# Kernel tuning notes

Measured on AMD Instinct MI355X. Metric: run time of the kernel, lower is better.

## Reference

```python
import jax, jax.numpy as jnp
import numpy as np
from jax import lax

EPS = 1e-5  # nn.BatchNorm2d default eps


def _binarize_act(x):
    # out = sign(x).detach() - clip(x).detach() + clip(x)  (STE)
    c = jnp.clip(x, -1.0, 1.0)
    return c + lax.stop_gradient(jnp.sign(x) - c)


def _binarize_weight(w):
    # w.data = w.fp.sign().add(0.01).sign()  -> {-1,+1}, zeros map to +1.
    # Autograd in torch sees identity wrt the parameter (data swap), i.e. STE.
    wb = jnp.sign(jnp.sign(w) + 0.01)
    return w + lax.stop_gradient(wb - w)


def setup_inputs() -> dict:
    key = jax.random.key(0)
    k1, k2, k3, k4 = jax.random.split(key, 4)
    N, Cin, Cout, H, W = 16, 32, 32, 256, 256
    return {
        "x": jax.random.normal(k1, (N, Cin, H, W), dtype=jnp.float32),
        "weight": jax.random.normal(k2, (Cout, Cin, 3, 3), dtype=jnp.float32),
        "gamma": jnp.ones((Cout,), dtype=jnp.float32),
        "beta": jnp.zeros((Cout,), dtype=jnp.float32),
        "running_mean": jax.random.normal(k3, (Cout,), dtype=jnp.float32) * 0.1,
        "running_var": jax.random.uniform(k4, (Cout,), dtype=jnp.float32) + 0.5,
    }


def reference(x, weight, gamma, beta, running_mean, running_var):
    xb = _binarize_act(x)
    wb = _binarize_weight(weight)
    # 3x3, stride 1, padding 1 -> SAME spatial size
    out = lax.conv_general_dilated(
        xb, wb,
        window_strides=(1, 1),
        padding=((1, 1), (1, 1)),
        dimension_numbers=("NCHW", "OIHW", "NCHW"),
    )
    # BatchNorm2d (inference form with running stats), then ReLU
    inv = gamma / jnp.sqrt(running_var + EPS)  # [C]
    out = out * inv[None, :, None, None] + (beta - running_mean * inv)[None, :, None, None]
    return jax.nn.relu(out)
```

## Files before the change

kernel.cpp:

```cpp
#include <hip/hip_runtime.h>
#include <stdint.h>

#define NB   16
#define CIN  32
#define COUT 32
#define HH   256
#define WW   256
#define HWSZ (HH * WW)
#define EPSV 1e-5f
#define TWD  264

typedef int v4i  __attribute__((ext_vector_type(4)));
typedef int v16i __attribute__((ext_vector_type(16)));

__global__ __launch_bounds__(288) void pack_w_kernel(
    const float* __restrict__ wt, const float* __restrict__ gamma,
    const float* __restrict__ beta, const float* __restrict__ rmean,
    const float* __restrict__ rvar, uint4* __restrict__ afrag,
    float* __restrict__ c0f) {
    __shared__ uint32_t pws[COUT * 9];
    const int j = threadIdx.x;
    if (j < COUT * 9) {
        const int o = j / 9, t = j % 9;
        uint32_t bits = 0;
#pragma unroll
        for (int c = 0; c < CIN; ++c)
            bits |= (wt[(o * CIN + c) * 9 + t] < 0.f) ? (1u << c) : 0u;
        pws[j] = bits;
    }
    __syncthreads();
    if (j < 64) {
        const int sh = (j & 32) >> 1;
#pragma unroll
        for (int t = 0; t < 9; ++t) {
            const uint32_t chunk = pws[(j & 31) * 9 + t] >> sh;
            uint32_t w[4];
#pragma unroll
            for (int k = 0; k < 4; ++k) {
                const uint32_t y = (((chunk >> (4 * k)) & 0xFu) * 0x204081u) & 0x01010101u;
                w[k] = (y * 0xFEu) | 0x01010101u;
            }
            afrag[t * 64 + j] = make_uint4(w[0], w[1], w[2], w[3]);
        }
    }
    {
        const int cls = j >> 5;
        const int o   = j & 31;
        const int rc = cls / 3, cc = cls % 3;
        int wsum = 0;
#pragma unroll
        for (int dh = 0; dh < 3; ++dh)
#pragma unroll
            for (int dw = 0; dw < 3; ++dw) {
                const bool bad = (rc == 0 && dh == 0) || (rc == 2 && dh == 2) ||
                                 (cc == 0 && dw == 0) || (cc == 2 && dw == 2);
                if (!bad) wsum += 32 - 2 * __popc(pws[o * 9 + dh * 3 + dw]);
            }
        const float inv = gamma[o] * rsqrtf(rvar[o] + EPSV);
        c0f[cls * 32 + o] = beta[o] - rmean[o] * inv - (float)wsum * inv;
        if (cls == 0) c0f[288 + o] = 2.0f * inv;
    }
}

__global__ __launch_bounds__(256, 6) void biconv_mfma(
    const uint32_t* __restrict__ x, const uint4* __restrict__ afrag,
    const float* __restrict__ c0f, float* __restrict__ out) {
    const uint32_t bid = blockIdx.x;
    const uint32_t wg  = ((bid & 7u) << 9) | (bid >> 3);
    const int n   = wg >> 8;
    const int h   = wg & 255;
    const int tid  = threadIdx.x;
    const int lane = tid & 63;
    const int wave = tid >> 6;

    __shared__ uint32_t tiles[3][TWD];
    __shared__ uint4    afsh[9 * 64];
    __shared__ float    csh[320];

    if (tid < 192) {
        const int r  = tid >> 6;
        const int q  = tid & 63;
        const int hr = h - 1 + r;
        uint32_t b0 = 0, b1 = 0, b2 = 0, b3 = 0;
        if (hr >= 0 && hr < HH) {
            const uint32_t* xp = x + (size_t)n * (CIN * HWSZ) + (size_t)hr * WW + (q << 2);
#pragma unroll
            for (int c = 0; c < CIN; ++c) {
                const uint4 v = *reinterpret_cast<const uint4*>(xp + (size_t)c * HWSZ);
                b0 |= (v.x >> 31) << c;
                b1 |= (v.y >> 31) << c;
                b2 |= (v.z >> 31) << c;
                b3 |= (v.w >> 31) << c;
            }
            b0 = ~b0; b1 = ~b1; b2 = ~b2; b3 = ~b3;
        }
        *reinterpret_cast<uint4*>(&tiles[r][(q << 2) + 4]) = make_uint4(b0, b1, b2, b3);
    } else {
        const int t2 = tid - 192;
#pragma unroll
        for (int k = 0; k < 9; ++k) afsh[t2 + 64 * k] = afrag[t2 + 64 * k];
#pragma unroll
        for (int k = 0; k < 5; ++k) csh[t2 + 64 * k] = c0f[t2 + 64 * k];
        if (t2 < 6) tiles[t2 >> 1][(t2 & 1) ? 260 : 3] = 0u;
    }
    __syncthreads();

    const int l31 = lane & 31;
    const int shv = (lane & 32) >> 1;
    const int og  = (lane >> 5) << 2;
    const int pA  = (wave << 6) + l31;
    const int pB  = pA + 32;

    v16i acc0 = {0}, acc1 = {0};
#pragma unroll
    for (int dh = 0; dh < 3; ++dh) {
        const uint32_t* trow = &tiles[dh][0];
#pragma unroll
        for (int dw = 0; dw < 3; ++dw) {
            const v4i a = *reinterpret_cast<const v4i*>(&afsh[(dh * 3 + dw) * 64 + lane]);
            const uint32_t hA = trow[pA + 3 + dw] >> shv;
            const uint32_t hB = trow[pB + 3 + dw] >> shv;
            v4i b;
            b.x = (int)((( hA        & 0xFu) * 0x204081u) & 0x01010101u);
            b.y = (int)((((hA >> 4)  & 0xFu) * 0x204081u) & 0x01010101u);
            b.z = (int)((((hA >> 8)  & 0xFu) * 0x204081u) & 0x01010101u);
            b.w = (int)((((hA >> 12) & 0xFu) * 0x204081u) & 0x01010101u);
            acc0 = __builtin_amdgcn_mfma_i32_32x32x32_i8(a, b, acc0, 0, 0, 0);
            b.x = (int)((( hB        & 0xFu) * 0x204081u) & 0x01010101u);
            b.y = (int)((((hB >> 4)  & 0xFu) * 0x204081u) & 0x01010101u);
            b.z = (int)((((hB >> 8)  & 0xFu) * 0x204081u) & 0x01010101u);
            b.w = (int)((((hB >> 12) & 0xFu) * 0x204081u) & 0x01010101u);
            acc1 = __builtin_amdgcn_mfma_i32_32x32x32_i8(a, b, acc1, 0, 0, 0);
        }
    }

    const int rc   = (h == 0) ? 0 : ((h == HH - 1) ? 2 : 1);
    const int ccA  = (pA == 0) ? 0 : ((pA == WW - 1) ? 2 : 1);
    const int ccB  = (pB == WW - 1) ? 2 : 1;
    const float* c0A = &csh[(rc * 3 + ccA) * 32];
    const float* c0B = &csh[(rc * 3 + ccB) * 32];
    const float* c1  = &csh[288];
    float* outp = out + (size_t)n * (COUT * HWSZ) + (size_t)h * WW;
#pragma unroll
    for (int e = 0; e < 16; ++e) {
        const int o = (e & 3) + ((e >> 2) << 3) + og;
        const float vA = fmaf((float)acc0[e], c1[o], c0A[o]);
        const float vB = fmaf((float)acc1[e], c1[o], c0B[o]);
        __builtin_nontemporal_store(vA > 0.f ? vA : 0.f, outp + (size_t)o * HWSZ + pA);
        __builtin_nontemporal_store(vB > 0.f ? vB : 0.f, outp + (size_t)o * HWSZ + pB);
    }
}

extern "C" void kernel_launch(void* const* d_in, const int* in_sizes, int n_in,
                              void* d_out, int out_size, void* d_ws, size_t ws_size,
                              hipStream_t stream) {
    const float* x     = (const float*)d_in[0];
    const float* wt    = (const float*)d_in[1];
    const float* gamma = (const float*)d_in[2];
    const float* beta  = (const float*)d_in[3];
    const float* rmean = (const float*)d_in[4];
    const float* rvar  = (const float*)d_in[5];
    float* out = (float*)d_out;

    uint4* afrag = (uint4*)d_ws;
    float* c0f   = (float*)((char*)d_ws + 9216);

    pack_w_kernel<<<dim3(1), dim3(288), 0, stream>>>(wt, gamma, beta, rmean,
                                                     rvar, afrag, c0f);
    biconv_mfma<<<dim3(NB * HH), dim3(256), 0, stream>>>(
        (const uint32_t*)x, afrag, c0f, out);
}
```

Measured before the change: 50.42 us.

## Process two output rows per block, sharing input tiles, and read weights from global

Each block now computes two output rows from four packed input rows, so each input row is loaded and bit-packed fewer times overall and half as many blocks are launched. All 256 threads pack input rows, and the weight fragments and BN constants are read straight from global/L1 instead of being staged in LDS. The sign convention is flipped (no bit inversion, negated scale and constant) to drop the NOT ops. Each wave now runs two passes of MFMA and epilogue, which lengthens per-block work and may raise register pressure.

```diff
diff --git a/kernel.cpp b/kernel.cpp
--- a/kernel.cpp
+++ b/kernel.cpp
@@ -57,8 +57,8 @@
                 if (!bad) wsum += 32 - 2 * __popc(pws[o * 9 + dh * 3 + dw]);
             }
         const float inv = gamma[o] * rsqrtf(rvar[o] + EPSV);
-        c0f[cls * 32 + o] = beta[o] - rmean[o] * inv - (float)wsum * inv;
-        if (cls == 0) c0f[288 + o] = 2.0f * inv;
+        c0f[cls * 32 + o] = beta[o] - rmean[o] * inv + (float)wsum * inv;
+        if (cls == 0) c0f[288 + o] = -2.0f * inv;
     }
 }
 
@@ -66,21 +66,21 @@
     const uint32_t* __restrict__ x, const uint4* __restrict__ afrag,
     const float* __restrict__ c0f, float* __restrict__ out) {
     const uint32_t bid = blockIdx.x;
-    const uint32_t wg  = ((bid & 7u) << 9) | (bid >> 3);
-    const int n   = wg >> 8;
-    const int h   = wg & 255;
+    const uint32_t wg  = ((bid & 7u) << 8) | (bid >> 3);
+    const int n   = wg >> 7;
+    const int h0  = (wg & 127) << 1;
     const int tid  = threadIdx.x;
     const int lane = tid & 63;
     const int wave = tid >> 6;
 
-    __shared__ uint32_t tiles[3][TWD];
-    __shared__ uint4    afsh[9 * 64];
-    __shared__ float    csh[320];
+    __shared__ uint32_t tiles[4][TWD];
 
-    if (tid < 192) {
+    if (tid < 8) tiles[tid >> 1][(tid & 1) ? 260 : 3] = 0u;
+
+    {
         const int r  = tid >> 6;
         const int q  = tid & 63;
-        const int hr = h - 1 + r;
+        const int hr = h0 - 1 + r;
         uint32_t b0 = 0, b1 = 0, b2 = 0, b3 = 0;
         if (hr >= 0 && hr < HH) {
             const uint32_t* xp = x + (size_t)n * (CIN * HWSZ) + (size_t)hr * WW + (q << 2);
@@ -92,62 +92,60 @@
                 b2 |= (v.z >> 31) << c;
                 b3 |= (v.w >> 31) << c;
             }
-            b0 = ~b0; b1 = ~b1; b2 = ~b2; b3 = ~b3;
         }
         *reinterpret_cast<uint4*>(&tiles[r][(q << 2) + 4]) = make_uint4(b0, b1, b2, b3);
-    } else {
-        const int t2 = tid - 192;
-#pragma unroll
-        for (int k = 0; k < 9; ++k) afsh[t2 + 64 * k] = afrag[t2 + 64 * k];
-#pragma unroll
-        for (int k = 0; k < 5; ++k) csh[t2 + 64 * k] = c0f[t2 + 64 * k];
-        if (t2 < 6) tiles[t2 >> 1][(t2 & 1) ? 260 : 3] = 0u;
     }
     __syncthreads();
 
-    const int l31 = lane & 31;
-    const int shv = (lane & 32) >> 1;
-    const int og  = (lane >> 5) << 2;
-    const int pA  = (wave << 6) + l31;
-    const int pB  = pA + 32;
+    const int l31  = lane & 31;
+    const int shv  = (lane & 32) >> 1;
+    const int og   = (lane >> 5) << 2;
+    const int rsel = wave >> 1;
+    const int wseg = (wave & 1) << 7;
 
-    v16i acc0 = {0}, acc1 = {0};
+    const int h  = h0 + rsel;
+    const int rc = (h == 0) ? 0 : ((h == HH - 1) ? 2 : 1);
+    const float* c1 = c0f + 288;
+    float* outn = out + (size_t)n * (COUT * HWSZ) + (size_t)h * WW;
+
 #pragma unroll
-    for (int dh = 0; dh < 3; ++dh) {
-        const uint32_t* trow = &tiles[dh][0];
+    for (int p = 0; p < 2; ++p) {
+        const int pA = wseg + (p << 6) + l31;
+        const int pB = pA + 32;
+        v16i acc0 = {0}, acc1 = {0};
 #pragma unroll
-        for (int dw = 0; dw < 3; ++dw) {
-            const v4i a = *reinterpret_cast<const v4i*>(&afsh[(dh * 3 + dw) * 64 + lane]);
-            const uint32_t hA = trow[pA + 3 + dw] >> shv;
-            const uint32_t hB = trow[pB + 3 + dw] >> shv;
-            v4i b;
-            b.x = (int)((( hA        & 0xFu) * 0x204081u) & 0x01010101u);
-            b.y = (int)((((hA >> 4)  & 0xFu) * 0x204081u) & 0x01010101u);
-            b.z = (int)((((hA >> 8)  & 0xFu) * 0x204081u) & 0x01010101u);
-            b.w = (int)((((hA >> 12) & 0xFu) * 0x204081u) & 0x01010101u);
-            acc0 = __builtin_amdgcn_mfma_i32_32x32x32_i8(a, b, acc0, 0, 0, 0);
-            b.x = (int)((( hB        & 0xFu) * 0x204081u) & 0x01010101u);
-            b.y = (int)((((hB >> 4)  & 0xFu) * 0x204081u) & 0x01010101u);
-            b.z = (int)((((hB >> 8)  & 0xFu) * 0x204081u) & 0x01010101u);
-            b.w = (int)((((hB >> 12) & 0xFu) * 0x204081u) & 0x01010101u);
-            acc1 = __builtin_amdgcn_mfma_i32_32x32x32_i8(a, b, acc1, 0, 0, 0);
+        for (int dh = 0; dh < 3; ++dh) {
+            const uint32_t* trow = &tiles[rsel + dh][0];
+#pragma unroll
+            for (int dw = 0; dw < 3; ++dw) {
+                const v4i a = *reinterpret_cast<const v4i*>(&afrag[(dh * 3 + dw) * 64 + lane]);
+                const uint32_t hA = trow[pA + 3 + dw] >> shv;
+                const uint32_t hB = trow[pB + 3 + dw] >> shv;
+                v4i b;
+                b.x = (int)((( hA        & 0xFu) * 0x204081u) & 0x01010101u);
+                b.y = (int)((((hA >> 4)  & 0xFu) * 0x204081u) & 0x01010101u);
+                b.z = (int)((((hA >> 8)  & 0xFu) * 0x204081u) & 0x01010101u);
+                b.w = (int)((((hA >> 12) & 0xFu) * 0x204081u) & 0x01010101u);
+                acc0 = __builtin_amdgcn_mfma_i32_32x32x32_i8(a, b, acc0, 0, 0, 0);
+                b.x = (int)((( hB        & 0xFu) * 0x204081u) & 0x01010101u);
+                b.y = (int)((((hB >> 4)  & 0xFu) * 0x204081u) & 0x01010101u);
+                b.z = (int)((((hB >> 8)  & 0xFu) * 0x204081u) & 0x01010101u);
+                b.w = (int)((((hB >> 12) & 0xFu) * 0x204081u) & 0x01010101u);
+                acc1 = __builtin_amdgcn_mfma_i32_32x32x32_i8(a, b, acc1, 0, 0, 0);
+            }
         }
-    }
-
-    const int rc   = (h == 0) ? 0 : ((h == HH - 1) ? 2 : 1);
-    const int ccA  = (pA == 0) ? 0 : ((pA == WW - 1) ? 2 : 1);
-    const int ccB  = (pB == WW - 1) ? 2 : 1;
-    const float* c0A = &csh[(rc * 3 + ccA) * 32];
-    const float* c0B = &csh[(rc * 3 + ccB) * 32];
-    const float* c1  = &csh[288];
-    float* outp = out + (size_t)n * (COUT * HWSZ) + (size_t)h * WW;
+        const int ccA = (pA == 0) ? 0 : ((pA == WW - 1) ? 2 : 1);
+        const int ccB = (pB == WW - 1) ? 2 : 1;
+        const float* c0A = c0f + (rc * 3 + ccA) * 32;
+        const float* c0B = c0f + (rc * 3 + ccB) * 32;
 #pragma unroll
-    for (int e = 0; e < 16; ++e) {
-        const int o = (e & 3) + ((e >> 2) << 3) + og;
-        const float vA = fmaf((float)acc0[e], c1[o], c0A[o]);
-        const float vB = fmaf((float)acc1[e], c1[o], c0B[o]);
-        __builtin_nontemporal_store(vA > 0.f ? vA : 0.f, outp + (size_t)o * HWSZ + pA);
-        __builtin_nontemporal_store(vB > 0.f ? vB : 0.f, outp + (size_t)o * HWSZ + pB);
+        for (int e = 0; e < 16; ++e) {
+            const int o = (e & 3) + ((e >> 2) << 3) + og;
+            const float vA = fmaf((float)acc0[e], c1[o], c0A[o]);
+            const float vB = fmaf((float)acc1[e], c1[o], c0B[o]);
+            __builtin_nontemporal_store(vA > 0.f ? vA : 0.f, outn + (size_t)o * HWSZ + pA);
+            __builtin_nontemporal_store(vB > 0.f ? vB : 0.f, outn + (size_t)o * HWSZ + pB);
+        }
     }
 }
 
@@ -167,6 +165,6 @@
 
     pack_w_kernel<<<dim3(1), dim3(288), 0, stream>>>(wt, gamma, beta, rmean,
                                                      rvar, afrag, c0f);
-    biconv_mfma<<<dim3(NB * HH), dim3(256), 0, stream>>>(
+    biconv_mfma<<<dim3(NB * HH / 2), dim3(256), 0, stream>>>(
         (const uint32_t*)x, afrag, c0f, out);
 }
```

After: 84.37 us. 67.3% more time.
